# Kernel tuning notes

Hardware: AMD Instinct MI355X
Metric: run time of the kernel (lower is better)

## Reference

```python
import jax, jax.numpy as jnp
import numpy as np

B, T_HIST, D, H = 32768, 50, 3, 512
FUTURE = 30


def gru_cell(x, h, W_ih, W_hh, b_ih, b_hh):
    # PyTorch GRU cell math: gates ordered (r, z, n)
    gi = x @ W_ih.T + b_ih          # [B, 3H]
    gh = h @ W_hh.T + b_hh          # [B, 3H]
    i_r, i_z, i_n = jnp.split(gi, 3, axis=-1)
    h_r, h_z, h_n = jnp.split(gh, 3, axis=-1)
    r = jax.nn.sigmoid(i_r + h_r)
    z = jax.nn.sigmoid(i_z + h_z)
    n = jnp.tanh(i_n + r * h_n)
    return (1.0 - z) * n + z * h


def setup_inputs() -> dict:
    key = jax.random.key(0)
    ks = jax.random.split(key, 20)
    s = 0.04  # ~1/sqrt(H), matches PyTorch uniform init scale
    def p(k, shape):
        return jax.random.normal(k, shape, dtype=jnp.float32) * s
    return {
        "x_input": jax.random.normal(ks[0], (B, T_HIST, D), dtype=jnp.float32),
        "future_len": FUTURE,
        # encoder GRU, layer 0 (input D) and layer 1 (input H)
        "enc_W_ih0": p(ks[1], (3 * H, D)), "enc_W_hh0": p(ks[2], (3 * H, H)),
        "enc_b_ih0": p(ks[3], (3 * H,)),  "enc_b_hh0": p(ks[4], (3 * H,)),
        "enc_W_ih1": p(ks[5], (3 * H, H)), "enc_W_hh1": p(ks[6], (3 * H, H)),
        "enc_b_ih1": p(ks[7], (3 * H,)),  "enc_b_hh1": p(ks[8], (3 * H,)),
        # decoder GRU, layer 0 (input D = output_dim) and layer 1
        "dec_W_ih0": p(ks[9], (3 * H, D)), "dec_W_hh0": p(ks[10], (3 * H, H)),
        "dec_b_ih0": p(ks[11], (3 * H,)), "dec_b_hh0": p(ks[12], (3 * H,)),
        "dec_W_ih1": p(ks[13], (3 * H, H)), "dec_W_hh1": p(ks[14], (3 * H, H)),
        "dec_b_ih1": p(ks[15], (3 * H,)), "dec_b_hh1": p(ks[16], (3 * H,)),
        # output projection
        "fc_W": p(ks[17], (D, H)), "fc_b": p(ks[18], (D,)),
    }


def reference(x_input, future_len,
              enc_W_ih0, enc_W_hh0, enc_b_ih0, enc_b_hh0,
              enc_W_ih1, enc_W_hh1, enc_b_ih1, enc_b_hh1,
              dec_W_ih0, dec_W_hh0, dec_b_ih0, dec_b_hh0,
              dec_W_ih1, dec_W_hh1, dec_b_ih1, dec_b_hh1,
              fc_W, fc_b):
    b = x_input.shape[0]
    h_init = jnp.zeros((b, H), dtype=x_input.dtype)

    # ---- encoder: 2-layer GRU over history (eval mode, no dropout) ----
    def enc_step(carry, x_t):
        h0, h1 = carry
        h0 = gru_cell(x_t, h0, enc_W_ih0, enc_W_hh0, enc_b_ih0, enc_b_hh0)
        h1 = gru_cell(h0, h1, enc_W_ih1, enc_W_hh1, enc_b_ih1, enc_b_hh1)
        return (h0, h1), None

    (h0, h1), _ = jax.lax.scan(enc_step, (h_init, h_init),
                               jnp.swapaxes(x_input, 0, 1))  # [T, B, D]

    def dec_step(carry, _):
        d0, d1, xin = carry
        d0 = gru_cell(xin, d0, dec_W_ih0, dec_W_hh0, dec_b_ih0, dec_b_hh0)
        d1 = gru_cell(d0, d1, dec_W_ih1, dec_W_hh1, dec_b_ih1, dec_b_hh1)
        pred = d1 @ fc_W.T + fc_b  # [B, D]
        return (d0, d1, pred), pred

    _, outs = jax.lax.scan(dec_step, (h0, h1, x_input[:, -1, :]),
                           None, length=future_len)  # [F, B, D]
    return jnp.swapaxes(outs, 0, 1)  # [B, F, D]
```

## Files before the change

### kernel.cpp

```cpp
#include <hip/hip_runtime.h>
#include <hip/hip_fp16.h>
#include <stdint.h>

typedef _Float16 h8 __attribute__((ext_vector_type(8)));
typedef float f4 __attribute__((ext_vector_type(4)));

#define DEV static __device__ __forceinline__

constexpr int BATCH  = 32768;
constexpr int HID    = 512;
constexpr int T_HIST = 50;
constexpr int FUT    = 30;
constexpr int BM = 256, BN = 32, BK = 64;

DEV void gl2lds16(const void* g, void* l) {
  __builtin_amdgcn_global_load_lds(
      (const __attribute__((address_space(1))) void*)g,
      (__attribute__((address_space(3))) void*)l,
      16, 0, 0);
}

DEV float sigm(float x)     { return 1.f / (1.f + __expf(-x)); }
DEV float tanhfast(float x) { return 1.f - 2.f / (__expf(2.f * x) + 1.f); }

__global__ void zero_fill(float4* __restrict__ p, int n4) {
  int i = blockIdx.x * 256 + threadIdx.x;
  if (i < n4) p[i] = float4{0.f, 0.f, 0.f, 0.f};
}

__global__ void pack_w(const float* __restrict__ Wa, const float* __restrict__ Wb,
                       _Float16* __restrict__ out, int KC) {
  int i = blockIdx.x * 256 + threadIdx.x;
  int total = 16 * KC * 3 * 32 * 64;
  if (i >= total) return;
  int k0  = i & 7;
  int k8s = (i >> 3) & 7;
  int n   = (i >> 6) & 31;
  int t   = i >> 11;
  int g   = t % 3;
  int t2  = t / 3;
  int kc  = t2 % KC;
  int nb  = t2 / KC;
  int k8  = k8s ^ (n & 7);
  int row = g * 512 + nb * 32 + n;
  int kg  = kc * 64 + k8 * 8 + k0;
  float v = (kg < 512) ? Wa[(size_t)row * 512 + kg] : Wb[(size_t)row * 512 + kg - 512];
  out[i] = (_Float16)v;
}

__global__ void pack_bias(const float* __restrict__ bih, const float* __restrict__ bhh,
                          float* __restrict__ out) {
  int j = blockIdx.x * 256 + threadIdx.x;
  if (j >= 512) return;
  out[j]        = bih[j]        + bhh[j];
  out[512 + j]  = bih[512 + j]  + bhh[512 + j];
  out[1024 + j] = bih[1024 + j];
  out[1536 + j] = bhh[1024 + j];
}

__global__ void pack_wx(const float* __restrict__ Wih, float* __restrict__ out) {
  int i = blockIdx.x * 256 + threadIdx.x;
  if (i >= 512 * 9) return;
  int j = i / 9, q = i % 9, g = q / 3, k = q % 3;
  out[i] = Wih[(size_t)(g * 512 + j) * 3 + k];
}

template <int KC, bool L0>
__launch_bounds__(256, L0 ? 3 : 2)
__global__ void gru_step(const _Float16* __restrict__ Bp,
                         const _Float16* __restrict__ Alo,
                         const _Float16* __restrict__ Ahi,
                         _Float16* __restrict__ hnew16,
                         const float* __restrict__ bias,
                         const float* __restrict__ Wx,
                         const float* __restrict__ xin,
                         int xstride) {
  __shared__ alignas(16) _Float16 sA[BM * BK];
  __shared__ alignas(16) _Float16 sB[3 * BN * BK];

  const int tid  = threadIdx.x;
  const int wave = tid >> 6;
  const int lane = tid & 63;
  const int quad = lane >> 4;
  const int l15  = lane & 15;
  const int L  = blockIdx.x;
  const int c  = L & 7;
  const int q  = L >> 3;
  const int cb = q & 15;
  const int rb = (c << 4) | (q >> 4);
  const int row0 = rb * BM;
  const int col0 = cb * BN;

  f4 acc_r[4][2]  = {};
  f4 acc_z[4][2]  = {};
  f4 acc_n0[4][2] = {};
  f4 acc_n1[4][2] = {};

  const _Float16* Bblk = Bp + (size_t)cb * KC * (3 * BN * BK);

  for (int kc = 0; kc < KC; ++kc) {
    const _Float16* Asrc = (KC == 16 && kc >= 8) ? Ahi : Alo;
    const int kb = (kc & 7) * BK;
#pragma unroll
    for (int i = 0; i < 8; ++i) {
      int ga = wave * 512 + i * 64 + lane;
      int m = ga >> 3, k8s = ga & 7;
      int k8l = k8s ^ (m & 7);
      gl2lds16(Asrc + (size_t)(row0 + m) * HID + kb + k8l * 8,
               &sA[(wave * 512 + i * 64) * 8]);
    }
    const _Float16* Bsrc = Bblk + (size_t)kc * (3 * BN * BK);
#pragma unroll
    for (int i = 0; i < 3; ++i) {
      int gb = wave * 192 + i * 64 + lane;
      gl2lds16(Bsrc + (size_t)gb * 8, &sB[(wave * 192 + i * 64) * 8]);
    }
    __syncthreads();
#pragma unroll
    for (int s = 0; s < 2; ++s) {
      const int sw = ((s * 4 + quad) ^ (l15 & 7)) * 8;
      h8 af[4];
#pragma unroll
      for (int mt = 0; mt < 4; ++mt)
        af[mt] = *(const h8*)&sA[(wave * 64 + mt * 16 + l15) * BK + sw];
#pragma unroll
      for (int nt = 0; nt < 2; ++nt) {
        const int nrow = nt * 16 + l15;
        h8 br = *(const h8*)&sB[(0 * BN + nrow) * BK + sw];
        h8 bz = *(const h8*)&sB[(1 * BN + nrow) * BK + sw];
        h8 bn = *(const h8*)&sB[(2 * BN + nrow) * BK + sw];
#pragma unroll
        for (int mt = 0; mt < 4; ++mt) {
          acc_r[mt][nt] = __builtin_amdgcn_mfma_f32_16x16x32_f16(af[mt], br, acc_r[mt][nt], 0, 0, 0);
          acc_z[mt][nt] = __builtin_amdgcn_mfma_f32_16x16x32_f16(af[mt], bz, acc_z[mt][nt], 0, 0, 0);
          if (L0 || kc >= 8)
            acc_n1[mt][nt] = __builtin_amdgcn_mfma_f32_16x16x32_f16(af[mt], bn, acc_n1[mt][nt], 0, 0, 0);
          else
            acc_n0[mt][nt] = __builtin_amdgcn_mfma_f32_16x16x32_f16(af[mt], bn, acc_n0[mt][nt], 0, 0, 0);
        }
      }
    }
    __syncthreads();
  }

  const _Float16* hold16 = L0 ? Alo : Ahi;
  float bR[2], bZ[2], bI[2], bH[2];
  float wx[2][9];
#pragma unroll
  for (int nt = 0; nt < 2; ++nt) {
    int j = col0 + nt * 16 + l15;
    bR[nt] = bias[j];
    bZ[nt] = bias[512 + j];
    bI[nt] = bias[1024 + j];
    bH[nt] = bias[1536 + j];
    if constexpr (L0) {
#pragma unroll
      for (int q2 = 0; q2 < 9; ++q2) wx[nt][q2] = Wx[j * 9 + q2];
    }
  }
#pragma unroll
  for (int mt = 0; mt < 4; ++mt) {
    float xv[4][3];
    if constexpr (L0) {
#pragma unroll
      for (int r = 0; r < 4; ++r) {
        int b = row0 + wave * 64 + mt * 16 + quad * 4 + r;
        const float* xp = xin + (size_t)b * xstride;
        xv[r][0] = xp[0]; xv[r][1] = xp[1]; xv[r][2] = xp[2];
      }
    }
#pragma unroll
    for (int r = 0; r < 4; ++r) {
      int b = row0 + wave * 64 + mt * 16 + quad * 4 + r;
#pragma unroll
      for (int nt = 0; nt < 2; ++nt) {
        int j = col0 + nt * 16 + l15;
        size_t idx = (size_t)b * HID + j;
        float rr = acc_r[mt][nt][r] + bR[nt];
        float zz = acc_z[mt][nt][r] + bZ[nt];
        float hn = acc_n1[mt][nt][r] + bH[nt];
        float in_;
        if constexpr (L0) {
          const float* w = wx[nt];
          rr += xv[r][0] * w[0] + xv[r][1] * w[1] + xv[r][2] * w[2];
          zz += xv[r][0] * w[3] + xv[r][1] * w[4] + xv[r][2] * w[5];
          in_ = bI[nt] + xv[r][0] * w[6] + xv[r][1] * w[7] + xv[r][2] * w[8];
        } else {
          in_ = acc_n0[mt][nt][r] + bI[nt];
        }
        float rg = sigm(rr);
        float zg = sigm(zz);
        float ng = tanhfast(in_ + rg * hn);
        float hp = (float)hold16[idx];
        float hv = (1.f - zg) * ng + zg * hp;
        hnew16[idx] = (_Float16)hv;
      }
    }
  }
}

__global__ __launch_bounds__(256) void fc_kernel(const _Float16* __restrict__ h,
                                                 const float* __restrict__ W,
                                                 const float* __restrict__ bfc,
                                                 float* __restrict__ out) {
  int wave = threadIdx.x >> 6, lane = threadIdx.x & 63;
  int b = blockIdx.x * 4 + wave;
  const h8* hp = (const h8*)(h + (size_t)b * 512);
  h8 a0 = hp[lane];
  float s[3];
#pragma unroll
  for (int d = 0; d < 3; ++d) {
    const float4* wp = (const float4*)(W + d * 512);
    float4 w0 = wp[lane * 2], w1 = wp[lane * 2 + 1];
    s[d] = (float)a0[0] * w0.x + (float)a0[1] * w0.y + (float)a0[2] * w0.z + (float)a0[3] * w0.w
         + (float)a0[4] * w1.x + (float)a0[5] * w1.y + (float)a0[6] * w1.z + (float)a0[7] * w1.w;
  }
#pragma unroll
  for (int d = 0; d < 3; ++d)
#pragma unroll
    for (int off = 32; off > 0; off >>= 1) s[d] += __shfl_xor(s[d], off, 64);
  if (lane == 0) {
    out[(size_t)b * 90 + 0] = s[0] + bfc[0];
    out[(size_t)b * 90 + 1] = s[1] + bfc[1];
    out[(size_t)b * 90 + 2] = s[2] + bfc[2];
  }
}

extern "C" void kernel_launch(void* const* d_in, const int* in_sizes, int n_in,
                              void* d_out, int out_size, void* d_ws, size_t ws_size,
                              hipStream_t stream) {
  (void)in_sizes; (void)n_in; (void)out_size; (void)ws_size;
  const float* x_input = (const float*)d_in[0];
  const float* eWih0 = (const float*)d_in[2];
  const float* eWhh0 = (const float*)d_in[3];
  const float* ebih0 = (const float*)d_in[4];
  const float* ebhh0 = (const float*)d_in[5];
  const float* eWih1 = (const float*)d_in[6];
  const float* eWhh1 = (const float*)d_in[7];
  const float* ebih1 = (const float*)d_in[8];
  const float* ebhh1 = (const float*)d_in[9];
  const float* dWih0 = (const float*)d_in[10];
  const float* dWhh0 = (const float*)d_in[11];
  const float* dbih0 = (const float*)d_in[12];
  const float* dbhh0 = (const float*)d_in[13];
  const float* dWih1 = (const float*)d_in[14];
  const float* dWhh1 = (const float*)d_in[15];
  const float* dbih1 = (const float*)d_in[16];
  const float* dbhh1 = (const float*)d_in[17];
  const float* fcW   = (const float*)d_in[18];
  const float* fcb   = (const float*)d_in[19];
  float* out = (float*)d_out;

  char* ws = (char*)d_ws;
  const size_t S16 = (size_t)BATCH * HID * 2;
  _Float16* h0h[2] = {(_Float16*)(ws),            (_Float16*)(ws + S16)};
  _Float16* h1h[2] = {(_Float16*)(ws + 2 * S16),  (_Float16*)(ws + 3 * S16)};
  char* p = ws + 4 * S16;
  const size_t W8  = (size_t)16 * 8  * 3 * 32 * 64 * 2;
  const size_t W16 = (size_t)16 * 16 * 3 * 32 * 64 * 2;
  _Float16* pkE0 = (_Float16*)p; p += W8;
  _Float16* pkE1 = (_Float16*)p; p += W16;
  _Float16* pkD0 = (_Float16*)p; p += W8;
  _Float16* pkD1 = (_Float16*)p; p += W16;
  float* bE0 = (float*)p; p += 2048 * 4;
  float* bE1 = (float*)p; p += 2048 * 4;
  float* bD0 = (float*)p; p += 2048 * 4;
  float* bD1 = (float*)p; p += 2048 * 4;
  float* wxE = (float*)p; p += 512 * 9 * 4;
  float* wxD = (float*)p; p += 512 * 9 * 4;

  pack_w<<<dim3(3072), 256, 0, stream>>>(eWhh0, eWhh0, pkE0, 8);
  pack_w<<<dim3(6144), 256, 0, stream>>>(eWih1, eWhh1, pkE1, 16);
  pack_w<<<dim3(3072), 256, 0, stream>>>(dWhh0, dWhh0, pkD0, 8);
  pack_w<<<dim3(6144), 256, 0, stream>>>(dWih1, dWhh1, pkD1, 16);
  pack_bias<<<2, 256, 0, stream>>>(ebih0, ebhh0, bE0);
  pack_bias<<<2, 256, 0, stream>>>(ebih1, ebhh1, bE1);
  pack_bias<<<2, 256, 0, stream>>>(dbih0, dbhh0, bD0);
  pack_bias<<<2, 256, 0, stream>>>(dbih1, dbhh1, bD1);
  pack_wx<<<18, 256, 0, stream>>>(eWih0, wxE);
  pack_wx<<<18, 256, 0, stream>>>(dWih0, wxD);

  {
    int n4 = (int)(S16 / 16);
    zero_fill<<<(n4 + 255) / 256, 256, 0, stream>>>((float4*)h0h[0], n4);
    zero_fill<<<(n4 + 255) / 256, 256, 0, stream>>>((float4*)h1h[0], n4);
  }

  dim3 grid(2048), blk(256);
  int p0 = 0, p1 = 0;
  for (int t = 0; t < T_HIST; ++t) {
    gru_step<8, true><<<grid, blk, 0, stream>>>(pkE0, h0h[p0], nullptr,
                                                h0h[1 - p0], bE0, wxE,
                                                x_input + (size_t)t * 3, 150);
    p0 ^= 1;
    gru_step<16, false><<<grid, blk, 0, stream>>>(pkE1, h0h[p0], h1h[p1],
                                                  h1h[1 - p1], bE1, nullptr, nullptr, 0);
    p1 ^= 1;
  }
  for (int t = 0; t < FUT; ++t) {
    const float* xp; int xs;
    if (t == 0) { xp = x_input + (size_t)49 * 3; xs = 150; }
    else        { xp = out + (size_t)(t - 1) * 3; xs = 90; }
    gru_step<8, true><<<grid, blk, 0, stream>>>(pkD0, h0h[p0], nullptr,
                                                h0h[1 - p0], bD0, wxD, xp, xs);
    p0 ^= 1;
    gru_step<16, false><<<grid, blk, 0, stream>>>(pkD1, h0h[p0], h1h[p1],
                                                  h1h[1 - p1], bD1, nullptr, nullptr, 0);
    p1 ^= 1;
    fc_kernel<<<8192, 256, 0, stream>>>(h1h[p1], fcW, fcb, out + (size_t)t * 3);
  }
}
```

Measured before the change: 15.15 ms.

## Double-buffer B tiles in LDS and load A fragments directly into registers

The GRU step GEMM no longer stages the A (hidden-state) tile through LDS. Each lane loads its MFMA A fragments straight from global memory into registers, while B (weights) is double-buffered in LDS. A ping-pong software pipeline with explicit vmcnt waits and barriers overlaps the next chunk's loads with the current chunk's MFMAs, removing the A-tile LDS traffic and the load-then-compute stalls. It costs more VGPRs (two sets of 8 h8 fragments), so launch bounds for layer 0 drop from 3 to 2 waves per SIMD, and the direct global A loads are less coalesced.

```diff
diff --git a/kernel.cpp b/kernel.cpp
--- a/kernel.cpp
+++ b/kernel.cpp
@@ -66,7 +66,7 @@
 }
 
 template <int KC, bool L0>
-__launch_bounds__(256, L0 ? 3 : 2)
+__launch_bounds__(256, 2)
 __global__ void gru_step(const _Float16* __restrict__ Bp,
                          const _Float16* __restrict__ Alo,
                          const _Float16* __restrict__ Ahi,
@@ -75,8 +75,7 @@
                          const float* __restrict__ Wx,
                          const float* __restrict__ xin,
                          int xstride) {
-  __shared__ alignas(16) _Float16 sA[BM * BK];
-  __shared__ alignas(16) _Float16 sB[3 * BN * BK];
+  __shared__ alignas(16) _Float16 sB[2][3 * BN * BK];
 
   const int tid  = threadIdx.x;
   const int wave = tid >> 6;
@@ -98,49 +97,72 @@
 
   const _Float16* Bblk = Bp + (size_t)cb * KC * (3 * BN * BK);
 
-  for (int kc = 0; kc < KC; ++kc) {
-    const _Float16* Asrc = (KC == 16 && kc >= 8) ? Ahi : Alo;
-    const int kb = (kc & 7) * BK;
-#pragma unroll
-    for (int i = 0; i < 8; ++i) {
-      int ga = wave * 512 + i * 64 + lane;
-      int m = ga >> 3, k8s = ga & 7;
-      int k8l = k8s ^ (m & 7);
-      gl2lds16(Asrc + (size_t)(row0 + m) * HID + kb + k8l * 8,
-               &sA[(wave * 512 + i * 64) * 8]);
-    }
-    const _Float16* Bsrc = Bblk + (size_t)kc * (3 * BN * BK);
+  auto stageB = [&](int kcs) {
+    const _Float16* Bsrc = Bblk + (size_t)kcs * (3 * BN * BK);
+    _Float16* dst = sB[kcs & 1];
 #pragma unroll
     for (int i = 0; i < 3; ++i) {
-      int gb = wave * 192 + i * 64 + lane;
-      gl2lds16(Bsrc + (size_t)gb * 8, &sB[(wave * 192 + i * 64) * 8]);
-    }
-    __syncthreads();
-#pragma unroll
-    for (int s = 0; s < 2; ++s) {
-      const int sw = ((s * 4 + quad) ^ (l15 & 7)) * 8;
-      h8 af[4];
-#pragma unroll
-      for (int mt = 0; mt < 4; ++mt)
-        af[mt] = *(const h8*)&sA[(wave * 64 + mt * 16 + l15) * BK + sw];
+      int off = wave * 192 + i * 64;
+      gl2lds16(Bsrc + (size_t)(off + lane) * 8, dst + (size_t)off * 8);
+    }
+  };
+  auto loadA = [&](int kcs, h8 (&tgt)[8]) {
+    const _Float16* Asrc = (KC == 16 && kcs >= 8) ? Ahi : Alo;
+    const int kb = (kcs & 7) * BK;
+#pragma unroll
+    for (int mt = 0; mt < 4; ++mt) {
+      const _Float16* rp = Asrc + (size_t)(row0 + wave * 64 + mt * 16 + l15) * HID + kb + quad * 8;
+#pragma unroll
+      for (int sk = 0; sk < 2; ++sk)
+        tgt[mt * 2 + sk] = *(const h8*)(rp + sk * 32);
+    }
+  };
+  auto compute = [&](int s, const h8 (&A)[8]) {
+    const _Float16* sBc = sB[s & 1];
+#pragma unroll
+    for (int sk = 0; sk < 2; ++sk) {
+      const int sw = ((sk * 4 + quad) ^ (l15 & 7)) * 8;
 #pragma unroll
       for (int nt = 0; nt < 2; ++nt) {
         const int nrow = nt * 16 + l15;
-        h8 br = *(const h8*)&sB[(0 * BN + nrow) * BK + sw];
-        h8 bz = *(const h8*)&sB[(1 * BN + nrow) * BK + sw];
-        h8 bn = *(const h8*)&sB[(2 * BN + nrow) * BK + sw];
+        h8 br = *(const h8*)&sBc[(0 * BN + nrow) * BK + sw];
+        h8 bz = *(const h8*)&sBc[(1 * BN + nrow) * BK + sw];
+        h8 bn = *(const h8*)&sBc[(2 * BN + nrow) * BK + sw];
 #pragma unroll
         for (int mt = 0; mt < 4; ++mt) {
-          acc_r[mt][nt] = __builtin_amdgcn_mfma_f32_16x16x32_f16(af[mt], br, acc_r[mt][nt], 0, 0, 0);
-          acc_z[mt][nt] = __builtin_amdgcn_mfma_f32_16x16x32_f16(af[mt], bz, acc_z[mt][nt], 0, 0, 0);
-          if (L0 || kc >= 8)
-            acc_n1[mt][nt] = __builtin_amdgcn_mfma_f32_16x16x32_f16(af[mt], bn, acc_n1[mt][nt], 0, 0, 0);
+          acc_r[mt][nt] = __builtin_amdgcn_mfma_f32_16x16x32_f16(A[mt * 2 + sk], br, acc_r[mt][nt], 0, 0, 0);
+          acc_z[mt][nt] = __builtin_amdgcn_mfma_f32_16x16x32_f16(A[mt * 2 + sk], bz, acc_z[mt][nt], 0, 0, 0);
+          if (L0 || s >= 8)
+            acc_n1[mt][nt] = __builtin_amdgcn_mfma_f32_16x16x32_f16(A[mt * 2 + sk], bn, acc_n1[mt][nt], 0, 0, 0);
           else
-            acc_n0[mt][nt] = __builtin_amdgcn_mfma_f32_16x16x32_f16(af[mt], bn, acc_n0[mt][nt], 0, 0, 0);
+            acc_n0[mt][nt] = __builtin_amdgcn_mfma_f32_16x16x32_f16(A[mt * 2 + sk], bn, acc_n0[mt][nt], 0, 0, 0);
         }
       }
     }
-    __syncthreads();
+  };
+
+  h8 Aa[8], Ab[8];
+  stageB(0); loadA(0, Aa);
+
+  for (int s = 0; s < KC; s += 2) {
+    stageB(s + 1); loadA(s + 1, Ab);
+    asm volatile("s_waitcnt vmcnt(11)" ::: "memory");
+    __builtin_amdgcn_s_barrier();
+    __builtin_amdgcn_sched_barrier(0);
+    compute(s, Aa);
+    __builtin_amdgcn_sched_barrier(0);
+    __builtin_amdgcn_s_barrier();
+    if (s + 2 < KC) {
+      stageB(s + 2); loadA(s + 2, Aa);
+      asm volatile("s_waitcnt vmcnt(11)" ::: "memory");
+    } else {
+      asm volatile("s_waitcnt vmcnt(0)" ::: "memory");
+    }
+    __builtin_amdgcn_s_barrier();
+    __builtin_amdgcn_sched_barrier(0);
+    compute(s + 1, Ab);
+    __builtin_amdgcn_sched_barrier(0);
+    __builtin_amdgcn_s_barrier();
   }
 
   const _Float16* hold16 = L0 ? Alo : Ahi;
```

New measurement: 21.16 ms. 1.4x slower.
